# Kernel optimization log

Measured on AMD Instinct MI355X. Metric: run time of the kernel, lower is better.

## Reference

```python
import jax, jax.numpy as jnp
import numpy as np

B, S, D = 4, 2048, 1024
E, F, K = 8, 4096, 2  # num_experts, mlp_dim, experts_per_token


def setup_inputs() -> dict:
    key = jax.random.key(0)
    ks = jax.random.split(key, 5)
    scale_d = 1.0 / np.sqrt(D)
    scale_f = 1.0 / np.sqrt(F)
    return {
        "x": jax.random.normal(ks[0], (B, S, D), dtype=jnp.float32),
        "gate_w": jax.random.normal(ks[1], (D, E), dtype=jnp.float32) * scale_d,
        "wi0": jax.random.normal(ks[2], (E, D, F), dtype=jnp.float32) * scale_d,
        "wi1": jax.random.normal(ks[3], (E, D, F), dtype=jnp.float32) * scale_d,
        "wo": jax.random.normal(ks[4], (E, F, D), dtype=jnp.float32) * scale_f,
    }


def reference(x, gate_w, wi0, wi1, wo):
    # Gating: [B,S,E] logits -> top-k values/indices -> softmax over the k selected
    gate_logits = jnp.einsum("bsd,de->bse", x, gate_w)
    topk_w, topk_idx = jax.lax.top_k(gate_logits, K)  # [B,S,K]
    topk_w = jax.nn.softmax(topk_w, axis=-1)

    num_experts = wi0.shape[0]
    out = jnp.zeros_like(x)
    # Faithful to the naive MoE loop: every expert MLP runs over all tokens,
    # output masked/weighted by the token's gate weight for that expert.
    for e in range(num_experts):
        w_e = jnp.sum((topk_idx == e) * topk_w, axis=-1)  # [B,S]
        h = jax.nn.silu(jnp.einsum("bsd,df->bsf", x, wi0[e])) * jnp.einsum(
            "bsd,df->bsf", x, wi1[e]
        )  # gated SiLU MLP intermediate [B,S,F]
        out = out + w_e[..., None] * jnp.einsum("bsf,fd->bsd", h, wo[e])
    return out
```

## Files before the change

kernel.cpp:

```cpp
#include <hip/hip_runtime.h>
#include <math.h>

#define TOKENS 8192
#define DDIM 1024
#define FDIM 4096
#define NEXP 8
#define CAP 8192
#define BM 128
#define BN 128
#define BK 32

typedef __bf16 bf16x8 __attribute__((ext_vector_type(8)));
typedef float f32x4 __attribute__((ext_vector_type(4)));

__device__ __forceinline__ unsigned short f2bf(float f) {
  union { float f; unsigned int u; } v; v.f = f;
  unsigned int u = v.u;
  return (unsigned short)((u + 0x7FFFu + ((u >> 16) & 1u)) >> 16);
}
__device__ __forceinline__ float bf2f(unsigned short h) {
  union { unsigned int u; float f; } v; v.u = ((unsigned int)h) << 16;
  return v.f;
}


__global__ void k_convert_x(const float* __restrict__ x, unsigned short* __restrict__ xb) {
  int i = (blockIdx.x * 256 + threadIdx.x) * 4;
  float4 v = *(const float4*)(x + i);
  ushort4 o;
  o.x = f2bf(v.x); o.y = f2bf(v.y); o.z = f2bf(v.z); o.w = f2bf(v.w);
  *(ushort4*)(xb + i) = o;
}

__global__ void k_tconv(const float* __restrict__ in, unsigned short* __restrict__ out,
                        int R, int C) {
  __shared__ float tile[32][33];
  size_t mat = (size_t)R * C;
  const float* src = in + (size_t)blockIdx.z * mat;
  unsigned short* dst = out + (size_t)blockIdx.z * mat;
  int c0 = blockIdx.x * 32, r0 = blockIdx.y * 32;
  int t = threadIdx.x;
#pragma unroll
  for (int i = 0; i < 4; ++i) {
    int lin = t + i * 256;
    int r = lin >> 5, c = lin & 31;
    tile[r][c] = src[(size_t)(r0 + r) * C + (c0 + c)];
  }
  __syncthreads();
#pragma unroll
  for (int i = 0; i < 4; ++i) {
    int lin = t + i * 256;
    int cc = lin >> 5, rr = lin & 31;
    dst[(size_t)(c0 + cc) * R + (r0 + rr)] = f2bf(tile[rr][cc]);
  }
}


__global__ void k_zero(int* __restrict__ counts) {
  if (threadIdx.x < NEXP) counts[threadIdx.x] = 0;
}

__global__ void k_gate(const float* __restrict__ x, const float* __restrict__ gw,
                       int* __restrict__ counts, int* __restrict__ tok_list,
                       float* __restrict__ wgt_list, int* __restrict__ tok_slot) {
  int wave = threadIdx.x >> 6, lane = threadIdx.x & 63;
  int t = blockIdx.x * 4 + wave;
  const float* xr = x + (size_t)t * DDIM;
  float acc[NEXP];
#pragma unroll
  for (int e = 0; e < NEXP; ++e) acc[e] = 0.f;
  for (int d = lane; d < DDIM; d += 64) {
    float xv = xr[d];
    const float* g = gw + d * NEXP;
#pragma unroll
    for (int e = 0; e < NEXP; ++e) acc[e] += xv * g[e];
  }
#pragma unroll
  for (int e = 0; e < NEXP; ++e) {
#pragma unroll
    for (int off = 32; off > 0; off >>= 1) acc[e] += __shfl_down(acc[e], off, 64);
  }
  if (lane == 0) {
    int e0 = 0; float v0 = acc[0];
#pragma unroll
    for (int e = 1; e < NEXP; ++e) if (acc[e] > v0) { v0 = acc[e]; e0 = e; }
    int e1 = -1; float v1 = -3.0e38f;
#pragma unroll
    for (int e = 0; e < NEXP; ++e) if (e != e0 && acc[e] > v1) { v1 = acc[e]; e1 = e; }
    float p1 = expf(v1 - v0);
    float s = 1.0f + p1;
    float w0 = 1.0f / s, w1 = p1 / s;
    int pos0 = atomicAdd(&counts[e0], 1);
    tok_list[e0 * CAP + pos0] = t;
    wgt_list[e0 * CAP + pos0] = w0;
    tok_slot[t * 2 + 0] = e0 * CAP + pos0;
    int pos1 = atomicAdd(&counts[e1], 1);
    tok_list[e1 * CAP + pos1] = t;
    wgt_list[e1 * CAP + pos1] = w1;
    tok_slot[t * 2 + 1] = e1 * CAP + pos1;
  }
}

__global__ void k_scan(const int* __restrict__ counts, int* __restrict__ bases) {
  if (threadIdx.x == 0) {
    int s = 0;
    for (int e = 0; e < NEXP; ++e) { bases[e] = s; s += counts[e]; }
  }
}


__global__ __launch_bounds__(256, 2) void k_gemm1(
    const unsigned short* __restrict__ xb, const unsigned short* __restrict__ w0t,
    const unsigned short* __restrict__ w1t, const int* __restrict__ counts,
    const int* __restrict__ bases, const int* __restrict__ tok_list,
    unsigned short* __restrict__ H) {
  int e = blockIdx.z, mt = blockIdx.y, nt = blockIdx.x;
  int cnt = counts[e];
  int m0 = mt * BM;
  if (m0 >= cnt) return;
  int mv = min(BM, cnt - m0);
  int gbase = bases[e] + m0;

  __shared__ __align__(16) unsigned short As[BM * BK];
  __shared__ __align__(16) unsigned short B0s[BN * BK];
  __shared__ __align__(16) unsigned short B1s[BN * BK];
  __shared__ int toks[BM];

  int t = threadIdx.x;
  if (t < BM) toks[t] = tok_list[e * CAP + m0 + min(t, mv - 1)];
  __syncthreads();

  int wid = t >> 6, lane = t & 63;
  int wm = (wid >> 1) * 64, wn = (wid & 1) * 64;
  int fr = lane & 15, fq = lane >> 4;

  f32x4 acc0[4][4], acc1[4][4];
#pragma unroll
  for (int mi = 0; mi < 4; ++mi)
#pragma unroll
    for (int ni = 0; ni < 4; ++ni)
#pragma unroll
      for (int r = 0; r < 4; ++r) { acc0[mi][ni][r] = 0.f; acc1[mi][ni][r] = 0.f; }

  const unsigned short* b0p = w0t + ((size_t)e * FDIM + nt * BN) * DDIM;
  const unsigned short* b1p = w1t + ((size_t)e * FDIM + nt * BN) * DDIM;

  for (int kt = 0; kt < DDIM; kt += BK) {
#pragma unroll
    for (int i = 0; i < 2; ++i) {
      int c = t + i * 256;
      int m = c >> 2, kc = (c & 3) * 8;
      uint4 va = *(const uint4*)(xb + (size_t)toks[m] * DDIM + kt + kc);
      *(uint4*)(As + m * BK + kc) = va;
      uint4 v0 = *(const uint4*)(b0p + (size_t)m * DDIM + kt + kc);
      *(uint4*)(B0s + m * BK + kc) = v0;
      uint4 v1 = *(const uint4*)(b1p + (size_t)m * DDIM + kt + kc);
      *(uint4*)(B1s + m * BK + kc) = v1;
    }
    __syncthreads();
    bf16x8 a[4], b0[4], b1[4];
#pragma unroll
    for (int mi = 0; mi < 4; ++mi)
      a[mi] = *(const bf16x8*)(As + (wm + mi * 16 + fr) * BK + fq * 8);
#pragma unroll
    for (int ni = 0; ni < 4; ++ni) {
      b0[ni] = *(const bf16x8*)(B0s + (wn + ni * 16 + fr) * BK + fq * 8);
      b1[ni] = *(const bf16x8*)(B1s + (wn + ni * 16 + fr) * BK + fq * 8);
    }
#pragma unroll
    for (int mi = 0; mi < 4; ++mi)
#pragma unroll
      for (int ni = 0; ni < 4; ++ni) {
        acc0[mi][ni] = __builtin_amdgcn_mfma_f32_16x16x32_bf16(a[mi], b0[ni], acc0[mi][ni], 0, 0, 0);
        acc1[mi][ni] = __builtin_amdgcn_mfma_f32_16x16x32_bf16(a[mi], b1[ni], acc1[mi][ni], 0, 0, 0);
      }
    __syncthreads();
  }

  int n0 = nt * BN + wn;
#pragma unroll
  for (int mi = 0; mi < 4; ++mi) {
    int mloc = wm + mi * 16 + fq * 4;
#pragma unroll
    for (int ni = 0; ni < 4; ++ni) {
      int col = n0 + ni * 16 + fr;
#pragma unroll
      for (int r = 0; r < 4; ++r) {
        int mrow = mloc + r;
        if (mrow < mv) {
          float g = acc0[mi][ni][r];
          float hv = (g / (1.0f + expf(-g))) * acc1[mi][ni][r];
          H[(size_t)(gbase + mrow) * FDIM + col] = f2bf(hv);
        }
      }
    }
  }
}


__global__ __launch_bounds__(256, 2) void k_gemm2(
    const unsigned short* __restrict__ H, const unsigned short* __restrict__ wot,
    const int* __restrict__ counts, const int* __restrict__ bases,
    unsigned short* __restrict__ O) {
  int e = blockIdx.z, mt = blockIdx.y, nt = blockIdx.x;
  int cnt = counts[e];
  int m0 = mt * BM;
  if (m0 >= cnt) return;
  int mv = min(BM, cnt - m0);
  int gbase = bases[e] + m0;

  __shared__ __align__(16) unsigned short As[BM * BK];
  __shared__ __align__(16) unsigned short Bs[BN * BK];

  int t = threadIdx.x;
  int wid = t >> 6, lane = t & 63;
  int wm = (wid >> 1) * 64, wn = (wid & 1) * 64;
  int fr = lane & 15, fq = lane >> 4;

  f32x4 acc[4][4];
#pragma unroll
  for (int mi = 0; mi < 4; ++mi)
#pragma unroll
    for (int ni = 0; ni < 4; ++ni)
#pragma unroll
      for (int r = 0; r < 4; ++r) acc[mi][ni][r] = 0.f;

  const unsigned short* bp = wot + ((size_t)e * DDIM + nt * BN) * FDIM;

  for (int kt = 0; kt < FDIM; kt += BK) {
#pragma unroll
    for (int i = 0; i < 2; ++i) {
      int c = t + i * 256;
      int m = c >> 2, kc = (c & 3) * 8;
      int arow = gbase + min(m, mv - 1);
      uint4 va = *(const uint4*)(H + (size_t)arow * FDIM + kt + kc);
      *(uint4*)(As + m * BK + kc) = va;
      uint4 vb = *(const uint4*)(bp + (size_t)m * FDIM + kt + kc);
      *(uint4*)(Bs + m * BK + kc) = vb;
    }
    __syncthreads();
    bf16x8 a[4], b[4];
#pragma unroll
    for (int mi = 0; mi < 4; ++mi)
      a[mi] = *(const bf16x8*)(As + (wm + mi * 16 + fr) * BK + fq * 8);
#pragma unroll
    for (int ni = 0; ni < 4; ++ni)
      b[ni] = *(const bf16x8*)(Bs + (wn + ni * 16 + fr) * BK + fq * 8);
#pragma unroll
    for (int mi = 0; mi < 4; ++mi)
#pragma unroll
      for (int ni = 0; ni < 4; ++ni)
        acc[mi][ni] = __builtin_amdgcn_mfma_f32_16x16x32_bf16(a[mi], b[ni], acc[mi][ni], 0, 0, 0);
    __syncthreads();
  }

  int n0 = nt * BN + wn;
#pragma unroll
  for (int mi = 0; mi < 4; ++mi) {
    int mloc = wm + mi * 16 + fq * 4;
#pragma unroll
    for (int ni = 0; ni < 4; ++ni) {
      int col = n0 + ni * 16 + fr;
#pragma unroll
      for (int r = 0; r < 4; ++r) {
        int mrow = mloc + r;
        if (mrow < mv)
          O[(size_t)(gbase + mrow) * DDIM + col] = f2bf(acc[mi][ni][r]);
      }
    }
  }
}


__global__ void k_combine(const unsigned short* __restrict__ O, const int* __restrict__ bases,
                          const int* __restrict__ tok_slot, const float* __restrict__ wgt_list,
                          float* __restrict__ out) {
  int t = blockIdx.x;
  int s0 = tok_slot[t * 2 + 0];
  int s1 = tok_slot[t * 2 + 1];
  int g0 = bases[s0 / CAP] + (s0 & (CAP - 1));
  int g1 = bases[s1 / CAP] + (s1 & (CAP - 1));
  float w0 = wgt_list[s0], w1 = wgt_list[s1];
  int d = threadIdx.x * 4;
  ushort4 a = *(const ushort4*)(O + (size_t)g0 * DDIM + d);
  ushort4 b = *(const ushort4*)(O + (size_t)g1 * DDIM + d);
  float4 r;
  r.x = w0 * bf2f(a.x) + w1 * bf2f(b.x);
  r.y = w0 * bf2f(a.y) + w1 * bf2f(b.y);
  r.z = w0 * bf2f(a.z) + w1 * bf2f(b.z);
  r.w = w0 * bf2f(a.w) + w1 * bf2f(b.w);
  *(float4*)(out + (size_t)t * DDIM + d) = r;
}


extern "C" void kernel_launch(void* const* d_in, const int* in_sizes, int n_in,
                              void* d_out, int out_size, void* d_ws, size_t ws_size,
                              hipStream_t stream) {
  const float* x   = (const float*)d_in[0];
  const float* gw  = (const float*)d_in[1];
  const float* wi0 = (const float*)d_in[2];
  const float* wi1 = (const float*)d_in[3];
  const float* wo  = (const float*)d_in[4];
  float* out = (float*)d_out;

  char* p = (char*)d_ws;
  unsigned short* xb  = (unsigned short*)p; p += (size_t)TOKENS * DDIM * 2;
  unsigned short* w0t = (unsigned short*)p; p += (size_t)NEXP * FDIM * DDIM * 2;
  unsigned short* w1t = (unsigned short*)p; p += (size_t)NEXP * FDIM * DDIM * 2;
  unsigned short* wot = (unsigned short*)p; p += (size_t)NEXP * DDIM * FDIM * 2;
  unsigned short* H   = (unsigned short*)p; p += (size_t)2 * TOKENS * FDIM * 2;
  unsigned short* O   = (unsigned short*)p; p += (size_t)2 * TOKENS * DDIM * 2;
  int*   counts   = (int*)p; p += 256;
  int*   bases    = (int*)p; p += 256;
  int*   tok_list = (int*)p; p += (size_t)NEXP * CAP * 4;
  float* wgt_list = (float*)p; p += (size_t)NEXP * CAP * 4;
  int*   tok_slot = (int*)p; p += (size_t)TOKENS * 2 * 4;

  k_convert_x<<<(TOKENS * DDIM) / 1024, 256, 0, stream>>>(x, xb);
  k_tconv<<<dim3(FDIM / 32, DDIM / 32, NEXP), 256, 0, stream>>>(wi0, w0t, DDIM, FDIM);
  k_tconv<<<dim3(FDIM / 32, DDIM / 32, NEXP), 256, 0, stream>>>(wi1, w1t, DDIM, FDIM);
  k_tconv<<<dim3(DDIM / 32, FDIM / 32, NEXP), 256, 0, stream>>>(wo, wot, FDIM, DDIM);

  k_zero<<<1, 64, 0, stream>>>(counts);
  k_gate<<<TOKENS / 4, 256, 0, stream>>>(x, gw, counts, tok_list, wgt_list, tok_slot);
  k_scan<<<1, 64, 0, stream>>>(counts, bases);

  k_gemm1<<<dim3(FDIM / BN, CAP / BM, NEXP), 256, 0, stream>>>(xb, w0t, w1t, counts, bases, tok_list, H);
  k_gemm2<<<dim3(DDIM / BN, CAP / BM, NEXP), 256, 0, stream>>>(H, wot, counts, bases, O);

  k_combine<<<TOKENS, 256, 0, stream>>>(O, bases, tok_slot, wgt_list, out);
}
```

Before: 1.317 ms.

## Use direct global-to-LDS loads with XOR swizzle and widen weight transpose tiles

Both expert GEMMs now stage A and B tiles with global_load_lds, which copies global memory straight into LDS and skips the register round-trip. An XOR swizzle on the 16-byte column chunk is applied on both write and read to cut LDS bank conflicts on the MFMA operand loads. The weight transpose-convert kernel moves to 32x128 tiles with float4 loads and ushort4 stores to improve coalescing. This relies on the exact lane-to-address mapping that global_load_lds requires, and the swizzle must stay consistent across the writers and readers.

```diff
diff --git a/kernel.cpp b/kernel.cpp
--- a/kernel.cpp
+++ b/kernel.cpp
@@ -23,6 +23,12 @@
   return v.f;
 }
 
+__device__ __forceinline__ void load_lds16(const void* g, void* l) {
+  __builtin_amdgcn_global_load_lds(
+      (const __attribute__((address_space(1))) void*)g,
+      (__attribute__((address_space(3))) void*)l, 16, 0, 0);
+}
+
 
 __global__ void k_convert_x(const float* __restrict__ x, unsigned short* __restrict__ xb) {
   int i = (blockIdx.x * 256 + threadIdx.x) * 4;
@@ -34,24 +40,30 @@
 
 __global__ void k_tconv(const float* __restrict__ in, unsigned short* __restrict__ out,
                         int R, int C) {
-  __shared__ float tile[32][33];
+  __shared__ float tile[32][132];
   size_t mat = (size_t)R * C;
   const float* src = in + (size_t)blockIdx.z * mat;
   unsigned short* dst = out + (size_t)blockIdx.z * mat;
-  int c0 = blockIdx.x * 32, r0 = blockIdx.y * 32;
+  int c0 = blockIdx.x * 128, r0 = blockIdx.y * 32;
   int t = threadIdx.x;
 #pragma unroll
   for (int i = 0; i < 4; ++i) {
-    int lin = t + i * 256;
-    int r = lin >> 5, c = lin & 31;
-    tile[r][c] = src[(size_t)(r0 + r) * C + (c0 + c)];
+    int idx = i * 1024 + t * 4;
+    int r = idx >> 7, c = idx & 127;
+    float4 v = *(const float4*)(src + (size_t)(r0 + r) * C + (c0 + c));
+    *(float4*)&tile[r][c] = v;
   }
   __syncthreads();
 #pragma unroll
   for (int i = 0; i < 4; ++i) {
-    int lin = t + i * 256;
-    int cc = lin >> 5, rr = lin & 31;
-    dst[(size_t)(c0 + cc) * R + (r0 + rr)] = f2bf(tile[rr][cc]);
+    int idx = i * 1024 + t * 4;
+    int c = idx >> 5, r = idx & 31;
+    ushort4 o;
+    o.x = f2bf(tile[r + 0][c]);
+    o.y = f2bf(tile[r + 1][c]);
+    o.z = f2bf(tile[r + 2][c]);
+    o.w = f2bf(tile[r + 3][c]);
+    *(ushort4*)(dst + (size_t)(c0 + c) * R + (r0 + r)) = o;
   }
 }
 
@@ -133,6 +145,11 @@
   int wid = t >> 6, lane = t & 63;
   int wm = (wid >> 1) * 64, wn = (wid & 1) * 64;
   int fr = lane & 15, fq = lane >> 4;
+  int csl = fq ^ ((fr >> 1) & 3);
+
+  int row0 = t >> 2,        row1 = (t + 256) >> 2;
+  int fq0 = (t & 3) ^ ((row0 >> 1) & 3);
+  int fq1 = ((t + 256) & 3) ^ ((row1 >> 1) & 3);
 
   f32x4 acc0[4][4], acc1[4][4];
 #pragma unroll
@@ -144,28 +161,25 @@
 
   const unsigned short* b0p = w0t + ((size_t)e * FDIM + nt * BN) * DDIM;
   const unsigned short* b1p = w1t + ((size_t)e * FDIM + nt * BN) * DDIM;
+  const size_t arow0 = (size_t)toks[row0] * DDIM;
+  const size_t arow1 = (size_t)toks[row1] * DDIM;
 
   for (int kt = 0; kt < DDIM; kt += BK) {
-#pragma unroll
-    for (int i = 0; i < 2; ++i) {
-      int c = t + i * 256;
-      int m = c >> 2, kc = (c & 3) * 8;
-      uint4 va = *(const uint4*)(xb + (size_t)toks[m] * DDIM + kt + kc);
-      *(uint4*)(As + m * BK + kc) = va;
-      uint4 v0 = *(const uint4*)(b0p + (size_t)m * DDIM + kt + kc);
-      *(uint4*)(B0s + m * BK + kc) = v0;
-      uint4 v1 = *(const uint4*)(b1p + (size_t)m * DDIM + kt + kc);
-      *(uint4*)(B1s + m * BK + kc) = v1;
-    }
+    load_lds16(xb + arow0 + kt + fq0 * 8, As + t * 8);
+    load_lds16(xb + arow1 + kt + fq1 * 8, As + (t + 256) * 8);
+    load_lds16(b0p + (size_t)row0 * DDIM + kt + fq0 * 8, B0s + t * 8);
+    load_lds16(b0p + (size_t)row1 * DDIM + kt + fq1 * 8, B0s + (t + 256) * 8);
+    load_lds16(b1p + (size_t)row0 * DDIM + kt + fq0 * 8, B1s + t * 8);
+    load_lds16(b1p + (size_t)row1 * DDIM + kt + fq1 * 8, B1s + (t + 256) * 8);
     __syncthreads();
     bf16x8 a[4], b0[4], b1[4];
 #pragma unroll
     for (int mi = 0; mi < 4; ++mi)
-      a[mi] = *(const bf16x8*)(As + (wm + mi * 16 + fr) * BK + fq * 8);
+      a[mi] = *(const bf16x8*)(As + (wm + mi * 16 + fr) * BK + csl * 8);
 #pragma unroll
     for (int ni = 0; ni < 4; ++ni) {
-      b0[ni] = *(const bf16x8*)(B0s + (wn + ni * 16 + fr) * BK + fq * 8);
-      b1[ni] = *(const bf16x8*)(B1s + (wn + ni * 16 + fr) * BK + fq * 8);
+      b0[ni] = *(const bf16x8*)(B0s + (wn + ni * 16 + fr) * BK + csl * 8);
+      b1[ni] = *(const bf16x8*)(B1s + (wn + ni * 16 + fr) * BK + csl * 8);
     }
 #pragma unroll
     for (int mi = 0; mi < 4; ++mi)
@@ -216,6 +230,11 @@
   int wid = t >> 6, lane = t & 63;
   int wm = (wid >> 1) * 64, wn = (wid & 1) * 64;
   int fr = lane & 15, fq = lane >> 4;
+  int csl = fq ^ ((fr >> 1) & 3);
+
+  int row0 = t >> 2,        row1 = (t + 256) >> 2;
+  int fq0 = (t & 3) ^ ((row0 >> 1) & 3);
+  int fq1 = ((t + 256) & 3) ^ ((row1 >> 1) & 3);
 
   f32x4 acc[4][4];
 #pragma unroll
@@ -226,26 +245,22 @@
       for (int r = 0; r < 4; ++r) acc[mi][ni][r] = 0.f;
 
   const unsigned short* bp = wot + ((size_t)e * DDIM + nt * BN) * FDIM;
+  const size_t arow0 = (size_t)(gbase + min(row0, mv - 1)) * FDIM;
+  const size_t arow1 = (size_t)(gbase + min(row1, mv - 1)) * FDIM;
 
   for (int kt = 0; kt < FDIM; kt += BK) {
-#pragma unroll
-    for (int i = 0; i < 2; ++i) {
-      int c = t + i * 256;
-      int m = c >> 2, kc = (c & 3) * 8;
-      int arow = gbase + min(m, mv - 1);
-      uint4 va = *(const uint4*)(H + (size_t)arow * FDIM + kt + kc);
-      *(uint4*)(As + m * BK + kc) = va;
-      uint4 vb = *(const uint4*)(bp + (size_t)m * FDIM + kt + kc);
-      *(uint4*)(Bs + m * BK + kc) = vb;
-    }
+    load_lds16(H + arow0 + kt + fq0 * 8, As + t * 8);
+    load_lds16(H + arow1 + kt + fq1 * 8, As + (t + 256) * 8);
+    load_lds16(bp + (size_t)row0 * FDIM + kt + fq0 * 8, Bs + t * 8);
+    load_lds16(bp + (size_t)row1 * FDIM + kt + fq1 * 8, Bs + (t + 256) * 8);
     __syncthreads();
     bf16x8 a[4], b[4];
 #pragma unroll
     for (int mi = 0; mi < 4; ++mi)
-      a[mi] = *(const bf16x8*)(As + (wm + mi * 16 + fr) * BK + fq * 8);
+      a[mi] = *(const bf16x8*)(As + (wm + mi * 16 + fr) * BK + csl * 8);
 #pragma unroll
     for (int ni = 0; ni < 4; ++ni)
-      b[ni] = *(const bf16x8*)(Bs + (wn + ni * 16 + fr) * BK + fq * 8);
+      b[ni] = *(const bf16x8*)(Bs + (wn + ni * 16 + fr) * BK + csl * 8);
 #pragma unroll
     for (int mi = 0; mi < 4; ++mi)
 #pragma unroll
@@ -317,9 +332,9 @@
   int*   tok_slot = (int*)p; p += (size_t)TOKENS * 2 * 4;
 
   k_convert_x<<<(TOKENS * DDIM) / 1024, 256, 0, stream>>>(x, xb);
-  k_tconv<<<dim3(FDIM / 32, DDIM / 32, NEXP), 256, 0, stream>>>(wi0, w0t, DDIM, FDIM);
-  k_tconv<<<dim3(FDIM / 32, DDIM / 32, NEXP), 256, 0, stream>>>(wi1, w1t, DDIM, FDIM);
-  k_tconv<<<dim3(DDIM / 32, FDIM / 32, NEXP), 256, 0, stream>>>(wo, wot, FDIM, DDIM);
+  k_tconv<<<dim3(FDIM / 128, DDIM / 32, NEXP), 256, 0, stream>>>(wi0, w0t, DDIM, FDIM);
+  k_tconv<<<dim3(FDIM / 128, DDIM / 32, NEXP), 256, 0, stream>>>(wi1, w1t, DDIM, FDIM);
+  k_tconv<<<dim3(DDIM / 128, FDIM / 32, NEXP), 256, 0, stream>>>(wo, wot, FDIM, DDIM);
 
   k_zero<<<1, 64, 0, stream>>>(counts);
   k_gate<<<TOKENS / 4, 256, 0, stream>>>(x, gw, counts, tok_list, wgt_list, tok_slot);
```

Result: faster. 1.267 ms (-3.8%).
